# Optimization experiments

Hardware: AMD Instinct MI355X
Metric: run time of the kernel (lower is better)

Reference implementation:

```python
import jax, jax.numpy as jnp
import numpy as np

DIM = 1536
HEADS = 12
HD = DIM // HEADS  # 128
F, H, W = 4, 22, 40
L = F * H * W      # 3520
B = 1
EPS = 1e-6
SCALE = 1.0 / (HD ** 0.5)


def _rope_angles(max_pos=1024, head_dim=HD):
    # Wan rope_params: three blocks for (F,H,W) axes, dims (d-4*(d//6), 2*(d//6), 2*(d//6))
    d6 = head_dim // 6
    dims = [head_dim - 4 * d6, 2 * d6, 2 * d6]  # 44, 42, 42
    parts = []
    pos = np.arange(max_pos, dtype=np.float64)
    for dp in dims:
        inv = 1.0 / (10000.0 ** (np.arange(0, dp, 2, dtype=np.float64) / dp))
        parts.append(np.outer(pos, inv))  # [1024, dp//2]
    return np.concatenate(parts, axis=1).astype(np.float32)  # [1024, 64]


def setup_inputs() -> dict:
    key = jax.random.key(0)
    ks = jax.random.split(key, 10)
    std = 0.02
    inp = {
        "x": jax.random.normal(ks[0], (B, L, DIM), jnp.float32),
        "seq_lens": jnp.full((B,), L, jnp.int32),
        "grid_sizes": jnp.array([[F, H, W]], jnp.int32),
        "freqs": jnp.asarray(_rope_angles()),
        "Wq": jax.random.normal(ks[1], (DIM, DIM), jnp.float32) * std,
        "bq": jnp.zeros((DIM,), jnp.float32),
        "Wk": jax.random.normal(ks[2], (DIM, DIM), jnp.float32) * std,
        "bk": jnp.zeros((DIM,), jnp.float32),
        "Wv": jax.random.normal(ks[3], (DIM, DIM), jnp.float32) * std,
        "bv": jnp.zeros((DIM,), jnp.float32),
        "Wo": jax.random.normal(ks[4], (DIM, DIM), jnp.float32) * std,
        "bo": jnp.zeros((DIM,), jnp.float32),
        "gq": jnp.ones((DIM,), jnp.float32),
        "gk": jnp.ones((DIM,), jnp.float32),
    }
    return inp


def _rmsnorm(x, g):
    return x * jax.lax.rsqrt(jnp.mean(x * x, axis=-1, keepdims=True) + EPS) * g


def _rope_apply(x, grid_sizes, freqs):
    # x: [B, L, n, d]; freqs: [1024, d//2] angles. 3D grid RoPE (interleaved complex pairs).
    c = x.shape[-1] // 2  # 64
    sf = c - 2 * (c // 3)  # 22 freq channels for F axis; 21 each for H, W
    ff, fh, fw = freqs[:, :sf], freqs[:, sf:sf + c // 3], freqs[:, sf + c // 3:]

    def per_sample(xb, g):  # xb: [L, n, d], g: [3]
        f, h, w = g[0], g[1], g[2]
        idx = jnp.arange(xb.shape[0])
        fi = idx // (h * w)
        hi = (idx // w) % h
        wi = idx % w
        ang = jnp.concatenate([ff[fi], fh[hi], fw[wi]], axis=-1)  # [L, c]
        cos = jnp.cos(ang)[:, None, :]
        sin = jnp.sin(ang)[:, None, :]
        xr = xb.reshape(xb.shape[0], xb.shape[1], c, 2)
        x0, x1 = xr[..., 0], xr[..., 1]
        out = jnp.stack([x0 * cos - x1 * sin, x0 * sin + x1 * cos], axis=-1)
        return out.reshape(xb.shape)

    return jax.vmap(per_sample)(x, grid_sizes)


def reference(x, seq_lens, grid_sizes, freqs, Wq, bq, Wk, bk, Wv, bv, Wo, bo, gq, gk):
    b, s = x.shape[0], x.shape[1]
    q = _rmsnorm(x @ Wq.T + bq, gq).reshape(b, s, HEADS, HD)
    k = _rmsnorm(x @ Wk.T + bk, gk).reshape(b, s, HEADS, HD)
    v = (x @ Wv.T + bv).reshape(b, s, HEADS, HD)
    q = _rope_apply(q, grid_sizes, freqs)
    k = _rope_apply(k, grid_sizes, freqs)
    # non-causal full attention (seq_lens == L here, no padding mask needed)
    scores = jnp.einsum('bqnd,bknd->bnqk', q, k) * SCALE
    attn = jax.nn.softmax(scores, axis=-1)
    out = jnp.einsum('bnqk,bknd->bqnd', attn, v).reshape(b, s, DIM)
    return out @ Wo.T + bo
```

## Files before the change

### kernel.cpp

```cpp
#include <hip/hip_runtime.h>
#include <hip/hip_bf16.h>
#include <cstdint>

#define DIM   1536
#define HEADS 12
#define HD    128
#define LSEQ  3520
#define MPAD  3584
#define NKV   55
#define EPSF  1e-6f
#define QSCL  0.12751729198891580f

typedef __attribute__((ext_vector_type(4))) float f32x4;
typedef __attribute__((ext_vector_type(8))) short bf16x8;

__device__ __forceinline__ void gload16(const void* g, void* l) {
  __builtin_amdgcn_global_load_lds(
      (const __attribute__((address_space(1))) void*)g,
      (__attribute__((address_space(3))) void*)l, 16, 0, 0);
}

__device__ __forceinline__ ushort f2bf(float f) {
  union { float f; unsigned u; } v; v.f = f;
  unsigned u = v.u;
  return (ushort)((u + 0x7FFFu + ((u >> 16) & 1u)) >> 16);
}

__device__ __forceinline__ float bf2f(ushort u) {
  union { unsigned u; float f; } v; v.u = ((unsigned)u) << 16;
  return v.f;
}

__global__ __launch_bounds__(256) void cast_all(const float* __restrict__ x,
    const float* __restrict__ Wq, const float* __restrict__ Wk,
    const float* __restrict__ Wv, const float* __restrict__ Wo,
    ushort* __restrict__ dst) {
  long e = ((long)blockIdx.x * 256 + threadIdx.x) * 8;
  const float* src;
  long off;
  if (e < (long)MPAD * DIM) {
    if (e >= (long)LSEQ * DIM) {
      *(bf16x8*)(dst + e) = (bf16x8)(short)0;
      return;
    }
    src = x; off = e;
  } else {
    long e2 = e - (long)MPAD * DIM;
    int wsel = (int)(e2 / ((long)DIM * DIM));
    off = e2 - (long)wsel * DIM * DIM;
    src = wsel == 0 ? Wq : (wsel == 1 ? Wk : (wsel == 2 ? Wv : Wo));
  }
  float4 a = *(const float4*)(src + off);
  float4 b = *(const float4*)(src + off + 4);
  bf16x8 o;
  o[0] = (short)f2bf(a.x); o[1] = (short)f2bf(a.y);
  o[2] = (short)f2bf(a.z); o[3] = (short)f2bf(a.w);
  o[4] = (short)f2bf(b.x); o[5] = (short)f2bf(b.y);
  o[6] = (short)f2bf(b.z); o[7] = (short)f2bf(b.w);
  *(bf16x8*)(dst + e) = o;
}

__global__ __launch_bounds__(256) void gemm_qkv(const ushort* __restrict__ A,
    const ushort* __restrict__ B3,
    const float* __restrict__ bq, const float* __restrict__ bk2, const float* __restrict__ bv2,
    ushort* __restrict__ qbb, ushort* __restrict__ kbb, ushort* __restrict__ vTt) {
  __shared__ ushort As[128 * 64];
  __shared__ ushort Bs[128 * 64];
  const int m0 = blockIdx.x * 128;
  const int n0g = blockIdx.y * 128;
  const int which = n0g / 1536;
  const int n0l = n0g - which * 1536;
  const int t = threadIdx.x;
  const int lane = t & 63;
  const int w = t >> 6;
  const int wr = w >> 1, wc = w & 1;
  const int sr = t >> 3;
  const int sc = t & 7;

  f32x4 acc[4][4];
#pragma unroll
  for (int i = 0; i < 4; ++i)
#pragma unroll
    for (int j = 0; j < 4; ++j) acc[i][j] = (f32x4)0.0f;

  const int arow = 64 * wr + (lane & 15);
  const int brow = 64 * wc + (lane & 15);

  for (int k0 = 0; k0 < DIM; k0 += 64) {
    __syncthreads();
#pragma unroll
    for (int i = 0; i < 4; ++i) {
      int row = sr + 32 * i;
      int cs = sc ^ (row & 7);
      gload16(A + (long)(m0 + row) * DIM + k0 + cs * 8, (char*)As + row * 128 + sc * 16);
      gload16(B3 + (long)(n0g + row) * DIM + k0 + cs * 8, (char*)Bs + row * 128 + sc * 16);
    }
    __syncthreads();
    bf16x8 af[4][2], bfr[4][2];
#pragma unroll
    for (int mi = 0; mi < 4; ++mi) {
      int row = arow + 16 * mi;
#pragma unroll
      for (int ks = 0; ks < 2; ++ks) {
        int ck = (ks * 4 + (lane >> 4)) ^ (row & 7);
        af[mi][ks] = *(const bf16x8*)(As + row * 64 + ck * 8);
      }
    }
#pragma unroll
    for (int ni = 0; ni < 4; ++ni) {
      int row = brow + 16 * ni;
#pragma unroll
      for (int ks = 0; ks < 2; ++ks) {
        int ck = (ks * 4 + (lane >> 4)) ^ (row & 7);
        bfr[ni][ks] = *(const bf16x8*)(Bs + row * 64 + ck * 8);
      }
    }
#pragma unroll
    for (int mi = 0; mi < 4; ++mi)
#pragma unroll
      for (int ni = 0; ni < 4; ++ni)
#pragma unroll
        for (int ks = 0; ks < 2; ++ks)
          acc[mi][ni] = __builtin_amdgcn_mfma_f32_16x16x32_bf16(
              af[mi][ks], bfr[ni][ks], acc[mi][ni], 0, 0, 0);
  }

  const float* bias = which == 0 ? bq : (which == 1 ? bk2 : bv2);
#pragma unroll
  for (int mi = 0; mi < 4; ++mi) {
#pragma unroll
    for (int ni = 0; ni < 4; ++ni) {
      int gmb = m0 + 64 * wr + 16 * mi + (lane >> 4) * 4;
      int gnl = n0l + 64 * wc + 16 * ni + (lane & 15);
      float bvv = bias[gnl];
      if (which == 2) {
        if (gmb < LSEQ) {
          ushort4 o;
          o.x = f2bf(acc[mi][ni][0] + bvv);
          o.y = f2bf(acc[mi][ni][1] + bvv);
          o.z = f2bf(acc[mi][ni][2] + bvv);
          o.w = f2bf(acc[mi][ni][3] + bvv);
          *(ushort4*)(vTt + (long)gnl * LSEQ + gmb) = o;
        }
      } else {
        ushort* dst = which ? kbb : qbb;
        if (gmb < LSEQ) {
#pragma unroll
          for (int j = 0; j < 4; ++j)
            dst[(long)(gmb + j) * DIM + gnl] = f2bf(acc[mi][ni][j] + bvv);
        }
      }
    }
  }
}

__global__ __launch_bounds__(256) void gemm_out(const ushort* __restrict__ A,
    const ushort* __restrict__ B, const float* __restrict__ bias,
    float* __restrict__ Cf) {
  __shared__ ushort As[128 * 64];
  __shared__ ushort Bs[128 * 64];
  const int m0 = blockIdx.x * 128;
  const int n0 = blockIdx.y * 128;
  const int t = threadIdx.x;
  const int lane = t & 63;
  const int w = t >> 6;
  const int wr = w >> 1, wc = w & 1;
  const int sr = t >> 3;
  const int sc = t & 7;

  f32x4 acc[4][4];
#pragma unroll
  for (int i = 0; i < 4; ++i)
#pragma unroll
    for (int j = 0; j < 4; ++j) acc[i][j] = (f32x4)0.0f;

  const int arow = 64 * wr + (lane & 15);
  const int brow = 64 * wc + (lane & 15);

  for (int k0 = 0; k0 < DIM; k0 += 64) {
    __syncthreads();
#pragma unroll
    for (int i = 0; i < 4; ++i) {
      int row = sr + 32 * i;
      int cs = sc ^ (row & 7);
      gload16(A + (long)(m0 + row) * DIM + k0 + cs * 8, (char*)As + row * 128 + sc * 16);
      gload16(B + (long)(n0 + row) * DIM + k0 + cs * 8, (char*)Bs + row * 128 + sc * 16);
    }
    __syncthreads();
    bf16x8 af[4][2], bfr[4][2];
#pragma unroll
    for (int mi = 0; mi < 4; ++mi) {
      int row = arow + 16 * mi;
#pragma unroll
      for (int ks = 0; ks < 2; ++ks) {
        int ck = (ks * 4 + (lane >> 4)) ^ (row & 7);
        af[mi][ks] = *(const bf16x8*)(As + row * 64 + ck * 8);
      }
    }
#pragma unroll
    for (int ni = 0; ni < 4; ++ni) {
      int row = brow + 16 * ni;
#pragma unroll
      for (int ks = 0; ks < 2; ++ks) {
        int ck = (ks * 4 + (lane >> 4)) ^ (row & 7);
        bfr[ni][ks] = *(const bf16x8*)(Bs + row * 64 + ck * 8);
      }
    }
#pragma unroll
    for (int mi = 0; mi < 4; ++mi)
#pragma unroll
      for (int ni = 0; ni < 4; ++ni)
#pragma unroll
        for (int ks = 0; ks < 2; ++ks)
          acc[mi][ni] = __builtin_amdgcn_mfma_f32_16x16x32_bf16(
              af[mi][ks], bfr[ni][ks], acc[mi][ni], 0, 0, 0);
  }

#pragma unroll
  for (int mi = 0; mi < 4; ++mi) {
#pragma unroll
    for (int ni = 0; ni < 4; ++ni) {
      int gmb = m0 + 64 * wr + 16 * mi + (lane >> 4) * 4;
      int gn  = n0 + 64 * wc + 16 * ni + (lane & 15);
      float bvv = bias[gn];
      if (gmb < LSEQ) {
#pragma unroll
        for (int j = 0; j < 4; ++j)
          Cf[(long)(gmb + j) * DIM + gn] = acc[mi][ni][j] + bvv;
      }
    }
  }
}

__global__ __launch_bounds__(256) void postqk_kernel(ushort* __restrict__ qb,
    ushort* __restrict__ kb, const float* __restrict__ gq_,
    const float* __restrict__ gk_, const float* __restrict__ freqs) {
  const int l = blockIdx.x;
  const int t = threadIdx.x;
  ushort* buf      = blockIdx.y ? kb : qb;
  const float* g   = blockIdx.y ? gk_ : gq_;
  const float post = blockIdx.y ? 1.0f : QSCL;
  ushort* row = buf + (long)l * DIM + t * 6;
  float v[6];
  {
    ushort2 p0 = *(const ushort2*)(row);
    ushort2 p1 = *(const ushort2*)(row + 2);
    ushort2 p2 = *(const ushort2*)(row + 4);
    v[0] = bf2f(p0.x); v[1] = bf2f(p0.y); v[2] = bf2f(p1.x);
    v[3] = bf2f(p1.y); v[4] = bf2f(p2.x); v[5] = bf2f(p2.y);
  }
  float ss = v[0]*v[0] + v[1]*v[1] + v[2]*v[2] + v[3]*v[3] + v[4]*v[4] + v[5]*v[5];
#pragma unroll
  for (int off = 1; off < 64; off <<= 1) ss += __shfl_xor(ss, off);
  __shared__ float red[4];
  if ((t & 63) == 0) red[t >> 6] = ss;
  __syncthreads();
  float scale = rsqrtf((red[0] + red[1] + red[2] + red[3]) * (1.0f / DIM) + EPSF) * post;
  const int fi = l / (22 * 40);
  const int hi = (l / 40) % 22;
  const int wi = l % 40;
  ushort o[6];
#pragma unroll
  for (int ii = 0; ii < 3; ++ii) {
    int pg = t * 3 + ii;
    int c = pg & 63;
    int rsel = (c < 22) ? fi : ((c < 43) ? hi : wi);
    float ang = freqs[rsel * 64 + c];
    float sn, cs;
    __sincosf(ang, &sn, &cs);
    float x0 = v[2*ii]   * scale * g[t*6 + 2*ii];
    float x1 = v[2*ii+1] * scale * g[t*6 + 2*ii+1];
    o[2*ii]   = f2bf(x0 * cs - x1 * sn);
    o[2*ii+1] = f2bf(x0 * sn + x1 * cs);
  }
  *(ushort2*)(row)     = make_ushort2(o[0], o[1]);
  *(ushort2*)(row + 2) = make_ushort2(o[2], o[3]);
  *(ushort2*)(row + 4) = make_ushort2(o[4], o[5]);
}

__global__ __launch_bounds__(256) void attn_kernel(const ushort* __restrict__ qb,
    const ushort* __restrict__ kb, const ushort* __restrict__ vT,
    ushort* __restrict__ ab) {
  __shared__ ushort KV[2][2][8192];
  __shared__ ushort Ps[4][16 * 72];
  const int qt = blockIdx.x;
  const int h  = blockIdx.y;
  const int t = threadIdx.x;
  const int lane = t & 63;
  const int w = t >> 6;
  const int q16 = lane & 15;
  const int hi = lane >> 4;

  auto stageKV = [&](int buf, int kv0) {
    int rr = t >> 4, ck = t & 15;
#pragma unroll
    for (int i = 0; i < 4; ++i) {
      int row = rr + 16 * i;
      int cs = ck ^ (row & 7);
      gload16(kb + (long)(kv0 + row) * DIM + h * HD + cs * 8,
              (char*)&KV[buf][0][0] + row * 256 + ck * 16);
    }
    int rv = t >> 3, cv = t & 7;
#pragma unroll
    for (int i = 0; i < 4; ++i) {
      int row = rv + 32 * i;
      int cs = cv ^ (row & 7);
      gload16(vT + (long)(h * HD + row) * LSEQ + kv0 + cs * 8,
              (char*)&KV[buf][1][0] + row * 128 + cv * 16);
    }
  };

  {
    int rr = t >> 4, ck = t & 15;
#pragma unroll
    for (int i = 0; i < 4; ++i) {
      int row = rr + 16 * i;
      int cs = ck ^ (row & 7);
      gload16(qb + (long)(qt * 64 + row) * DIM + h * HD + cs * 8,
              (char*)&KV[1][0][0] + row * 256 + ck * 16);
    }
  }
  stageKV(0, 0);
  asm volatile("s_waitcnt vmcnt(8)" ::: "memory");
  __builtin_amdgcn_s_barrier();

  bf16x8 aq[4];
  {
    int row = 16 * w + q16;
#pragma unroll
    for (int ks = 0; ks < 4; ++ks) {
      int ck = (ks * 4 + hi) ^ (row & 7);
      aq[ks] = *(const bf16x8*)((const char*)&KV[1][0][0] + row * 256 + ck * 16);
    }
  }
  asm volatile("s_waitcnt lgkmcnt(0)" ::: "memory");
  __builtin_amdgcn_s_barrier();

  f32x4 acc_o[8];
#pragma unroll
  for (int i = 0; i < 8; ++i) acc_o[i] = (f32x4)0.0f;
  float m_r = -1e30f, l_r = 0.0f;

  auto compute = [&](int buf) {
    const ushort* Ks = &KV[buf][0][0];
    const ushort* Vs = &KV[buf][1][0];
    f32x4 s[4];
#pragma unroll
    for (int nf = 0; nf < 4; ++nf) {
      s[nf] = (f32x4)0.0f;
      int row = 16 * nf + q16;
#pragma unroll
      for (int ks = 0; ks < 4; ++ks) {
        int ck = (ks * 4 + hi) ^ (row & 7);
        bf16x8 bk = *(const bf16x8*)(Ks + row * 128 + ck * 8);
        s[nf] = __builtin_amdgcn_mfma_f32_16x16x32_bf16(bk, aq[ks], s[nf], 0, 0, 0);
      }
    }
    float mx = s[0][0];
#pragma unroll
    for (int nf = 0; nf < 4; ++nf)
#pragma unroll
      for (int j = 0; j < 4; ++j) mx = fmaxf(mx, s[nf][j]);
    mx = fmaxf(mx, __shfl_xor(mx, 16));
    mx = fmaxf(mx, __shfl_xor(mx, 32));
    float mnew = fmaxf(m_r, mx);
    float fj = exp2f(m_r - mnew);
    float p[16], rs = 0.0f;
#pragma unroll
    for (int nf = 0; nf < 4; ++nf)
#pragma unroll
      for (int j = 0; j < 4; ++j) {
        float pv = exp2f(s[nf][j] - mnew);
        p[nf * 4 + j] = pv;
        rs += pv;
      }
    rs += __shfl_xor(rs, 16);
    rs += __shfl_xor(rs, 32);
    l_r = l_r * fj + rs;
    m_r = mnew;
#pragma unroll
    for (int ni = 0; ni < 8; ++ni) acc_o[ni] *= fj;
#pragma unroll
    for (int nf = 0; nf < 4; ++nf) {
      ushort4 o;
      o.x = f2bf(p[nf * 4 + 0]);
      o.y = f2bf(p[nf * 4 + 1]);
      o.z = f2bf(p[nf * 4 + 2]);
      o.w = f2bf(p[nf * 4 + 3]);
      *(ushort4*)(&Ps[w][q16 * 72 + nf * 16 + hi * 4]) = o;
    }
#pragma unroll
    for (int ks = 0; ks < 2; ++ks) {
      bf16x8 ap = *(const bf16x8*)(&Ps[w][q16 * 72 + ks * 32 + hi * 8]);
#pragma unroll
      for (int ni = 0; ni < 8; ++ni) {
        int row = 16 * ni + q16;
        int ck = (ks * 4 + hi) ^ (row & 7);
        bf16x8 bv = *(const bf16x8*)(Vs + row * 64 + ck * 8);
        acc_o[ni] = __builtin_amdgcn_mfma_f32_16x16x32_bf16(bv, ap, acc_o[ni], 0, 0, 0);
      }
    }
  };

  for (int tt = 0; tt < NKV - 1; ++tt) {
    stageKV((tt + 1) & 1, (tt + 1) * 64);
    asm volatile("s_waitcnt vmcnt(8)" ::: "memory");
    __builtin_amdgcn_s_barrier();
    compute(tt & 1);
    __builtin_amdgcn_s_barrier();
  }
  asm volatile("s_waitcnt vmcnt(0)" ::: "memory");
  __builtin_amdgcn_s_barrier();
  compute((NKV - 1) & 1);

  float inv_l = 1.0f / l_r;
  const int qg = qt * 64 + 16 * w + q16;
#pragma unroll
  for (int ni = 0; ni < 8; ++ni) {
    ushort4 o;
    o.x = f2bf(acc_o[ni][0] * inv_l);
    o.y = f2bf(acc_o[ni][1] * inv_l);
    o.z = f2bf(acc_o[ni][2] * inv_l);
    o.w = f2bf(acc_o[ni][3] * inv_l);
    *(ushort4*)(ab + (long)qg * DIM + h * HD + 16 * ni + hi * 4) = o;
  }
}

extern "C" void kernel_launch(void* const* d_in, const int* in_sizes, int n_in,
                              void* d_out, int out_size, void* d_ws, size_t ws_size,
                              hipStream_t stream) {
  const float* x     = (const float*)d_in[0];
  const float* freqs = (const float*)d_in[3];
  const float* Wq = (const float*)d_in[4];  const float* bq = (const float*)d_in[5];
  const float* Wk = (const float*)d_in[6];  const float* bk = (const float*)d_in[7];
  const float* Wv = (const float*)d_in[8];  const float* bv = (const float*)d_in[9];
  const float* Wo = (const float*)d_in[10]; const float* bo = (const float*)d_in[11];
  const float* gq = (const float*)d_in[12]; const float* gk = (const float*)d_in[13];

  char* ws = (char*)d_ws;
  size_t off = 0;
  auto alloc = [&](size_t bytes) -> char* {
    char* p = ws + off;
    off += (bytes + 255) & ~(size_t)255;
    return p;
  };
  ushort* xb   = (ushort*)alloc((size_t)MPAD * DIM * 2 + 4 * (size_t)DIM * DIM * 2);
  ushort* wall = xb + (size_t)MPAD * DIM;
  ushort* wob  = wall + 3 * (size_t)DIM * DIM;
  ushort* qbb = (ushort*)alloc((size_t)LSEQ * DIM * 2);
  ushort* kbb = (ushort*)alloc((size_t)LSEQ * DIM * 2);
  ushort* vT  = (ushort*)alloc((size_t)DIM * LSEQ * 2);
  ushort* ab  = (ushort*)alloc((size_t)MPAD * DIM * 2);

  const long tot8 = ((long)MPAD * DIM + 4L * DIM * DIM) / 8;
  cast_all<<<(int)(tot8 / 256), 256, 0, stream>>>(x, Wq, Wk, Wv, Wo, xb);

  gemm_qkv<<<dim3(MPAD / 128, 36), 256, 0, stream>>>(xb, wall, bq, bk, bv, qbb, kbb, vT);

  postqk_kernel<<<dim3(LSEQ, 2), 256, 0, stream>>>(qbb, kbb, gq, gk, freqs);

  attn_kernel<<<dim3(NKV, HEADS), 256, 0, stream>>>(qbb, kbb, vT, ab);

  gemm_out<<<dim3(MPAD / 128, DIM / 128), 256, 0, stream>>>(ab, wob, bo, (float*)d_out);
}
```

Before: 436.5 us.

## Split attention waves 2x2 over query/key halves with lazy rescale and combine

Restructures the attention kernel so each wave handles 32 query rows and half of each 64-key tile, reusing every K and V fragment load for two MFMAs. The two key-split waves keep separate softmax states and merge them at the end through shared memory. It also skips the online-softmax rescale when the running max grows by no more than 8 (log2 units), uses the hardware exp2 and packed bf16 conversion, and raises wave priority around the MFMA loops. The cost is more registers for the doubled accumulators and an extra cross-wave reduction step at the end.

```diff
diff --git a/kernel.cpp b/kernel.cpp
--- a/kernel.cpp
+++ b/kernel.cpp
@@ -29,6 +29,18 @@
 __device__ __forceinline__ float bf2f(ushort u) {
   union { unsigned u; float f; } v; v.u = ((unsigned)u) << 16;
   return v.f;
+}
+
+#if __has_builtin(__builtin_amdgcn_exp2f)
+__device__ __forceinline__ float ex2(float x) { return __builtin_amdgcn_exp2f(x); }
+#else
+__device__ __forceinline__ float ex2(float x) { return exp2f(x); }
+#endif
+
+__device__ __forceinline__ unsigned cvtpk(float a, float b) {
+  unsigned r;
+  asm("v_cvt_pk_bf16_f32 %0, %1, %2" : "=v"(r) : "v"(a), "v"(b));
+  return r;
 }
 
 __global__ __launch_bounds__(256) void cast_all(const float* __restrict__ x,
@@ -282,12 +294,15 @@
     const ushort* __restrict__ kb, const ushort* __restrict__ vT,
     ushort* __restrict__ ab) {
   __shared__ ushort KV[2][2][8192];
-  __shared__ ushort Ps[4][16 * 72];
+  __shared__ ushort Ps[4][32 * 40];
+  __shared__ float2 Msh[4][2][16];
   const int qt = blockIdx.x;
   const int h  = blockIdx.y;
   const int t = threadIdx.x;
   const int lane = t & 63;
   const int w = t >> 6;
+  const int a = w >> 1;
+  const int b = w & 1;
   const int q16 = lane & 15;
   const int hi = lane >> 4;
 
@@ -324,82 +339,99 @@
   asm volatile("s_waitcnt vmcnt(8)" ::: "memory");
   __builtin_amdgcn_s_barrier();
 
-  bf16x8 aq[4];
-  {
-    int row = 16 * w + q16;
+  bf16x8 aq[2][4];
+#pragma unroll
+  for (int qf = 0; qf < 2; ++qf) {
+    int row = a * 32 + qf * 16 + q16;
 #pragma unroll
     for (int ks = 0; ks < 4; ++ks) {
       int ck = (ks * 4 + hi) ^ (row & 7);
-      aq[ks] = *(const bf16x8*)((const char*)&KV[1][0][0] + row * 256 + ck * 16);
+      aq[qf][ks] = *(const bf16x8*)((const char*)&KV[1][0][0] + row * 256 + ck * 16);
     }
   }
   asm volatile("s_waitcnt lgkmcnt(0)" ::: "memory");
   __builtin_amdgcn_s_barrier();
 
-  f32x4 acc_o[8];
-#pragma unroll
-  for (int i = 0; i < 8; ++i) acc_o[i] = (f32x4)0.0f;
-  float m_r = -1e30f, l_r = 0.0f;
+  f32x4 acc[8][2];
+#pragma unroll
+  for (int i = 0; i < 8; ++i) { acc[i][0] = (f32x4)0.0f; acc[i][1] = (f32x4)0.0f; }
+  float m_r[2] = {-1e30f, -1e30f};
+  float l_r[2] = {0.f, 0.f};
+  ushort* Psw = &Ps[w][0];
 
   auto compute = [&](int buf) {
     const ushort* Ks = &KV[buf][0][0];
     const ushort* Vs = &KV[buf][1][0];
-    f32x4 s[4];
-#pragma unroll
-    for (int nf = 0; nf < 4; ++nf) {
-      s[nf] = (f32x4)0.0f;
-      int row = 16 * nf + q16;
+    f32x4 s[2][2];
+    s[0][0] = (f32x4)0.0f; s[0][1] = (f32x4)0.0f;
+    s[1][0] = (f32x4)0.0f; s[1][1] = (f32x4)0.0f;
+    __builtin_amdgcn_s_setprio(1);
+#pragma unroll
+    for (int kf = 0; kf < 2; ++kf) {
+      int krow = b * 32 + kf * 16 + q16;
 #pragma unroll
       for (int ks = 0; ks < 4; ++ks) {
-        int ck = (ks * 4 + hi) ^ (row & 7);
-        bf16x8 bk = *(const bf16x8*)(Ks + row * 128 + ck * 8);
-        s[nf] = __builtin_amdgcn_mfma_f32_16x16x32_bf16(bk, aq[ks], s[nf], 0, 0, 0);
-      }
-    }
-    float mx = s[0][0];
-#pragma unroll
-    for (int nf = 0; nf < 4; ++nf)
-#pragma unroll
-      for (int j = 0; j < 4; ++j) mx = fmaxf(mx, s[nf][j]);
-    mx = fmaxf(mx, __shfl_xor(mx, 16));
-    mx = fmaxf(mx, __shfl_xor(mx, 32));
-    float mnew = fmaxf(m_r, mx);
-    float fj = exp2f(m_r - mnew);
-    float p[16], rs = 0.0f;
-#pragma unroll
-    for (int nf = 0; nf < 4; ++nf)
-#pragma unroll
-      for (int j = 0; j < 4; ++j) {
-        float pv = exp2f(s[nf][j] - mnew);
-        p[nf * 4 + j] = pv;
-        rs += pv;
-      }
-    rs += __shfl_xor(rs, 16);
-    rs += __shfl_xor(rs, 32);
-    l_r = l_r * fj + rs;
-    m_r = mnew;
-#pragma unroll
-    for (int ni = 0; ni < 8; ++ni) acc_o[ni] *= fj;
-#pragma unroll
-    for (int nf = 0; nf < 4; ++nf) {
-      ushort4 o;
-      o.x = f2bf(p[nf * 4 + 0]);
-      o.y = f2bf(p[nf * 4 + 1]);
-      o.z = f2bf(p[nf * 4 + 2]);
-      o.w = f2bf(p[nf * 4 + 3]);
-      *(ushort4*)(&Ps[w][q16 * 72 + nf * 16 + hi * 4]) = o;
-    }
-#pragma unroll
-    for (int ks = 0; ks < 2; ++ks) {
-      bf16x8 ap = *(const bf16x8*)(&Ps[w][q16 * 72 + ks * 32 + hi * 8]);
-#pragma unroll
-      for (int ni = 0; ni < 8; ++ni) {
-        int row = 16 * ni + q16;
-        int ck = (ks * 4 + hi) ^ (row & 7);
-        bf16x8 bv = *(const bf16x8*)(Vs + row * 64 + ck * 8);
-        acc_o[ni] = __builtin_amdgcn_mfma_f32_16x16x32_bf16(bv, ap, acc_o[ni], 0, 0, 0);
-      }
-    }
+        int ck = (ks * 4 + hi) ^ (krow & 7);
+        bf16x8 kk = *(const bf16x8*)(Ks + krow * 128 + ck * 8);
+        s[kf][0] = __builtin_amdgcn_mfma_f32_16x16x32_bf16(kk, aq[0][ks], s[kf][0], 0, 0, 0);
+        s[kf][1] = __builtin_amdgcn_mfma_f32_16x16x32_bf16(kk, aq[1][ks], s[kf][1], 0, 0, 0);
+      }
+    }
+    __builtin_amdgcn_s_setprio(0);
+    float mx[2];
+#pragma unroll
+    for (int qf = 0; qf < 2; ++qf) {
+      float m01 = fmaxf(fmaxf(s[0][qf][0], s[0][qf][1]), s[0][qf][2]);
+      m01 = fmaxf(fmaxf(m01, s[0][qf][3]), s[1][qf][0]);
+      m01 = fmaxf(fmaxf(m01, s[1][qf][1]), s[1][qf][2]);
+      m01 = fmaxf(m01, s[1][qf][3]);
+      m01 = fmaxf(m01, __shfl_xor(m01, 16));
+      mx[qf] = fmaxf(m01, __shfl_xor(m01, 32));
+    }
+    bool noskip = !__all((mx[0] <= m_r[0] + 8.0f) & (mx[1] <= m_r[1] + 8.0f));
+    if (noskip) {
+#pragma unroll
+      for (int qf = 0; qf < 2; ++qf) {
+        float mnew = fmaxf(m_r[qf], mx[qf]);
+        float fj = ex2(m_r[qf] - mnew);
+        l_r[qf] *= fj;
+        m_r[qf] = mnew;
+#pragma unroll
+        for (int ni = 0; ni < 8; ++ni) acc[ni][qf] *= fj;
+      }
+    }
+#pragma unroll
+    for (int qf = 0; qf < 2; ++qf) {
+      float rs = 0.0f;
+#pragma unroll
+      for (int kf = 0; kf < 2; ++kf) {
+        float p0 = ex2(s[kf][qf][0] - m_r[qf]);
+        float p1 = ex2(s[kf][qf][1] - m_r[qf]);
+        float p2 = ex2(s[kf][qf][2] - m_r[qf]);
+        float p3 = ex2(s[kf][qf][3] - m_r[qf]);
+        rs += (p0 + p1) + (p2 + p3);
+        uint2 u;
+        u.x = cvtpk(p0, p1);
+        u.y = cvtpk(p2, p3);
+        *(uint2*)(&Psw[(qf * 16 + q16) * 40 + kf * 16 + hi * 4]) = u;
+      }
+      rs += __shfl_xor(rs, 16);
+      rs += __shfl_xor(rs, 32);
+      l_r[qf] += rs;
+    }
+    bf16x8 pf[2];
+    pf[0] = *(const bf16x8*)(&Psw[(0 * 16 + q16) * 40 + hi * 8]);
+    pf[1] = *(const bf16x8*)(&Psw[(1 * 16 + q16) * 40 + hi * 8]);
+    __builtin_amdgcn_s_setprio(1);
+#pragma unroll
+    for (int ni = 0; ni < 8; ++ni) {
+      int vrow = 16 * ni + q16;
+      int ck = (4 * b + hi) ^ (vrow & 7);
+      bf16x8 vv = *(const bf16x8*)(Vs + vrow * 64 + ck * 8);
+      acc[ni][0] = __builtin_amdgcn_mfma_f32_16x16x32_bf16(vv, pf[0], acc[ni][0], 0, 0, 0);
+      acc[ni][1] = __builtin_amdgcn_mfma_f32_16x16x32_bf16(vv, pf[1], acc[ni][1], 0, 0, 0);
+    }
+    __builtin_amdgcn_s_setprio(0);
   };
 
   for (int tt = 0; tt < NKV - 1; ++tt) {
@@ -413,16 +445,46 @@
   __builtin_amdgcn_s_barrier();
   compute((NKV - 1) & 1);
 
-  float inv_l = 1.0f / l_r;
-  const int qg = qt * 64 + 16 * w + q16;
+  __syncthreads();
+  if (hi < 2) Msh[w][hi][q16] = make_float2(m_r[hi], l_r[hi]);
+  __syncthreads();
+  float invl[2], fown[2];
+#pragma unroll
+  for (int qf = 0; qf < 2; ++qf) {
+    float2 pm = Msh[w ^ 1][qf][q16];
+    float ms = fmaxf(m_r[qf], pm.x);
+    fown[qf] = ex2(m_r[qf] - ms);
+    float ls = l_r[qf] * fown[qf] + pm.y * ex2(pm.x - ms);
+    invl[qf] = 1.0f / ls;
+  }
 #pragma unroll
   for (int ni = 0; ni < 8; ++ni) {
-    ushort4 o;
-    o.x = f2bf(acc_o[ni][0] * inv_l);
-    o.y = f2bf(acc_o[ni][1] * inv_l);
-    o.z = f2bf(acc_o[ni][2] * inv_l);
-    o.w = f2bf(acc_o[ni][3] * inv_l);
-    *(ushort4*)(ab + (long)qg * DIM + h * HD + 16 * ni + hi * 4) = o;
+    acc[ni][0] *= fown[0];
+    acc[ni][1] *= fown[1];
+  }
+  char* xch = (char*)&KV[0][0][0] + a * 17408 + lane * 272;
+  if (b == 1) {
+#pragma unroll
+    for (int ni = 0; ni < 8; ++ni) {
+      *(f32x4*)(xch + (ni * 2 + 0) * 16) = acc[ni][0];
+      *(f32x4*)(xch + (ni * 2 + 1) * 16) = acc[ni][1];
+    }
+  }
+  __syncthreads();
+  if (b == 0) {
+#pragma unroll
+    for (int ni = 0; ni < 8; ++ni) {
+#pragma unroll
+      for (int qf = 0; qf < 2; ++qf) {
+        f32x4 o = acc[ni][qf] + *(const f32x4*)(xch + (ni * 2 + qf) * 16);
+        float il = invl[qf];
+        uint2 pk;
+        pk.x = cvtpk(o[0] * il, o[1] * il);
+        pk.y = cvtpk(o[2] * il, o[3] * il);
+        int qrow = qt * 64 + a * 32 + qf * 16 + q16;
+        *(uint2*)(ab + (long)qrow * DIM + h * HD + 16 * ni + hi * 4) = pk;
+      }
+    }
   }
 }
 
```

New measurement: 403.4 us. 7.6% less time.
